# Performance work log

Hardware: AMD Instinct MI355X
Metric: run time of the kernel (lower is better)

The kernel has to match this reference:

```python
import jax, jax.numpy as jnp
import numpy as np

NUM_HEADS = 32
NUM_KV_HEADS = 8
HEAD_DIM = 128
ATTN_SCALE = 0.08838834764831845  # 1/sqrt(128)
CONTEXT_LEN = 8192
BLOCK_SIZE = 16
NUM_BLOCKS = 1024  # physical blocks -> 16384 cache slots


def setup_inputs() -> dict:
    key = jax.random.key(0)
    ks = jax.random.split(key, 6)
    q = jax.random.normal(ks[0], (1, NUM_HEADS, HEAD_DIM), jnp.float32)
    k = jax.random.normal(ks[1], (1, NUM_KV_HEADS, HEAD_DIM), jnp.float32)
    v = jax.random.normal(ks[2], (1, NUM_KV_HEADS, HEAD_DIM), jnp.float32)
    num_slots = NUM_BLOCKS * BLOCK_SIZE
    k_cache = jax.random.normal(ks[3], (num_slots, NUM_KV_HEADS, HEAD_DIM), jnp.float32)
    v_cache = jax.random.normal(ks[4], (num_slots, NUM_KV_HEADS, HEAD_DIM), jnp.float32)
    num_logical = CONTEXT_LEN // BLOCK_SIZE
    block_table = jax.random.permutation(ks[5], NUM_BLOCKS)[:num_logical].astype(jnp.int32)
    # new token is written at logical position context_len - 1
    last = CONTEXT_LEN - 1
    slot_mapping = (block_table[last // BLOCK_SIZE] * BLOCK_SIZE + last % BLOCK_SIZE)[None].astype(jnp.int32)
    return {"q": q, "k": k, "v": v, "k_cache": k_cache, "v_cache": v_cache,
            "block_table": block_table, "slot_mapping": slot_mapping,
            "context_len": CONTEXT_LEN, "block_size": BLOCK_SIZE}


def reference(q, k, v, k_cache, v_cache, block_table, slot_mapping, context_len, block_size):
    # _write_to_cache: scatter the new token's K/V into the paged cache
    k_cache = k_cache.at[slot_mapping].set(k)
    v_cache = v_cache.at[slot_mapping].set(v)
    # _build_full_slot_mapping + _read_from_cache: gather full context K/V
    pos = jnp.arange(context_len)
    slots = block_table[pos // block_size] * block_size + pos % block_size  # (S,)
    k_all = k_cache[slots]  # (S, Hkv, D)
    v_all = v_cache[slots]
    # GQA: repeat_interleave KV heads to match query heads
    g = NUM_HEADS // NUM_KV_HEADS
    k_all = jnp.repeat(k_all, g, axis=1)  # (S, H, D)
    v_all = jnp.repeat(v_all, g, axis=1)
    # manual masked SDPA; num_query_tokens == 1 -> mask is all-ones (no tril)
    scores = jnp.einsum('qhd,khd->hqk', q, k_all) * ATTN_SCALE  # (H, 1, S)
    weights = jax.nn.softmax(scores, axis=-1)
    out = jnp.einsum('hqk,khd->qhd', weights, v_all)  # (1, H, D)
    return out
```

## Files before the change

### kernel.cpp

```cpp
#include <hip/hip_runtime.h>
#include <math.h>


#define NUM_HEADS    32
#define NUM_KV_HEADS 8
#define GQA          4
#define HEAD_DIM     128
#define ATTN_SCALE   0.08838834764831845f
#define CTX          8192
#define BLK          16
#define SPLITS       256
#define HALVES       16
#define SG           8
#define SPS          (SPLITS / SG)

template<int CTRL>
__device__ __forceinline__ float dpp_add(float x) {
    int xi = __builtin_bit_cast(int, x);
    int yi = __builtin_amdgcn_update_dpp(xi, xi, CTRL, 0xF, 0xF, true);
    return x + __builtin_bit_cast(float, yi);
}
__device__ __forceinline__ float swz_add_x16(float x) {
    int yi = __builtin_amdgcn_ds_swizzle(__builtin_bit_cast(int, x), 0x401F);
    return x + __builtin_bit_cast(float, yi);
}
__device__ __forceinline__ float half_wave_sum(float s) {
    s = dpp_add<0xB1>(s);
    s = dpp_add<0x4E>(s);
    s = dpp_add<0x124>(s);
    s = dpp_add<0x128>(s);
    s = swz_add_x16(s);
    return s;
}

__global__ __launch_bounds__(512, 4) void attn_partial(
    const float* __restrict__ q,
    const float* __restrict__ knew,
    const float* __restrict__ vnew,
    const float* __restrict__ kc,
    const float* __restrict__ vc,
    const int*   __restrict__ bt,
    float*       __restrict__ o_part,
    float*       __restrict__ l_part)
{
    const int split = blockIdx.x;
    const int kvh   = blockIdx.y;
    const int tid   = threadIdx.x;
    const int halfid = tid >> 5;
    const int l      = tid & 31;

    const int b0 = bt[split * 2];
    const int b1 = bt[split * 2 + 1];

    float4 qf[GQA];
#pragma unroll
    for (int h = 0; h < GQA; ++h)
        qf[h] = *(const float4*)(q + (kvh * GQA + h) * HEAD_DIM + l * 4);

    float4 kf[2], vf[2];
#pragma unroll
    for (int j = 0; j < 2; ++j) {
        const int off = halfid * 2 + j;
        const int pg  = (off >> 4) ? b1 : b0;
        const float* kptr;
        const float* vptr;
        if (split == SPLITS - 1 && off == 31) {
            kptr = knew + kvh * HEAD_DIM;
            vptr = vnew + kvh * HEAD_DIM;
        } else {
            const size_t row = (((size_t)pg * BLK + (off & 15)) * NUM_KV_HEADS + kvh)
                               * HEAD_DIM;
            kptr = kc + row;
            vptr = vc + row;
        }
        kf[j] = *(const float4*)(kptr + l * 4);
        vf[j] = *(const float4*)(vptr + l * 4);
    }

    float s[2][GQA];
#pragma unroll
    for (int j = 0; j < 2; ++j)
#pragma unroll
        for (int h = 0; h < GQA; ++h)
            s[j][h] = qf[h].x * kf[j].x + qf[h].y * kf[j].y +
                      qf[h].z * kf[j].z + qf[h].w * kf[j].w;

#pragma unroll
    for (int j = 0; j < 2; ++j)
#pragma unroll
        for (int h = 0; h < GQA; ++h)
            s[j][h] = half_wave_sum(s[j][h]);

    float  lsum[GQA];
    float4 o[GQA];
#pragma unroll
    for (int h = 0; h < GQA; ++h) {
        const float p0 = __expf(s[0][h] * ATTN_SCALE);
        const float p1 = __expf(s[1][h] * ATTN_SCALE);
        lsum[h] = p0 + p1;
        o[h].x = p0 * vf[0].x + p1 * vf[1].x;
        o[h].y = p0 * vf[0].y + p1 * vf[1].y;
        o[h].z = p0 * vf[0].z + p1 * vf[1].z;
        o[h].w = p0 * vf[0].w + p1 * vf[1].w;
    }

    __shared__ float  lds_o[HALVES][GQA][HEAD_DIM];
    __shared__ float4 lds_l[HALVES];

#pragma unroll
    for (int h = 0; h < GQA; ++h)
        *(float4*)&lds_o[halfid][h][l * 4] = o[h];
    if (l == 0)
        lds_l[halfid] = make_float4(lsum[0], lsum[1], lsum[2], lsum[3]);
    __syncthreads();

    if (tid < HEAD_DIM) {
        const int d = tid;
#pragma unroll
        for (int h = 0; h < GQA; ++h) {
            float acc = 0.f;
#pragma unroll
            for (int i = 0; i < HALVES; ++i) acc += lds_o[i][h][d];
            o_part[((size_t)(kvh * GQA + h) * SPLITS + split) * HEAD_DIM + d] = acc;
        }
    } else if (tid < 128 + GQA) {
        const int h = tid - 128;
        const float* lp = (const float*)lds_l;
        float L = 0.f;
#pragma unroll
        for (int i = 0; i < HALVES; ++i) L += lp[i * 4 + h];
        l_part[(kvh * GQA + h) * SPLITS + split] = L;
    }
}

__global__ __launch_bounds__(128) void attn_reduce1(
    const float* __restrict__ o_part,
    const float* __restrict__ l_part,
    float*       __restrict__ o2,
    float*       __restrict__ l2)
{
    const int h  = blockIdx.x;
    const int sg = blockIdx.y;
    const int d  = threadIdx.x;
    const int s0 = sg * SPS;

    float acc = 0.f;
#pragma unroll 8
    for (int s = 0; s < SPS; ++s)
        acc += o_part[((size_t)h * SPLITS + s0 + s) * HEAD_DIM + d];
    o2[((size_t)h * SG + sg) * HEAD_DIM + d] = acc;

    if (d < SPS) {
        float lv = l_part[h * SPLITS + s0 + d];
#pragma unroll
        for (int off = 16; off >= 1; off >>= 1) lv += __shfl_xor(lv, off, 64);
        if (d == 0) l2[h * SG + sg] = lv;
    }
}

__global__ __launch_bounds__(128) void attn_reduce2(
    const float* __restrict__ o2,
    const float* __restrict__ l2,
    float*       __restrict__ out)
{
    const int h = blockIdx.x;
    const int d = threadIdx.x;

    float L = 0.f;
#pragma unroll
    for (int i = 0; i < SG; ++i) L += l2[h * SG + i];

    float acc = 0.f;
#pragma unroll
    for (int i = 0; i < SG; ++i)
        acc += o2[((size_t)h * SG + i) * HEAD_DIM + d];

    out[h * HEAD_DIM + d] = acc / L;
}

extern "C" void kernel_launch(void* const* d_in, const int* in_sizes, int n_in,
                              void* d_out, int out_size, void* d_ws, size_t ws_size,
                              hipStream_t stream) {
    const float* q    = (const float*)d_in[0];
    const float* knew = (const float*)d_in[1];
    const float* vnew = (const float*)d_in[2];
    const float* kc   = (const float*)d_in[3];
    const float* vc   = (const float*)d_in[4];
    const int*   bt   = (const int*)d_in[5];

    char* ws = (char*)d_ws;
    float* o_part = (float*)ws;
    ws += (size_t)NUM_HEADS * SPLITS * HEAD_DIM * sizeof(float);
    float* l_part = (float*)ws;
    ws += (size_t)NUM_HEADS * SPLITS * sizeof(float);
    float* o2     = (float*)ws;
    ws += (size_t)NUM_HEADS * SG * HEAD_DIM * sizeof(float);
    float* l2     = (float*)ws;

    attn_partial<<<dim3(SPLITS, NUM_KV_HEADS), 512, 0, stream>>>(
        q, knew, vnew, kc, vc, bt, o_part, l_part);
    attn_reduce1<<<dim3(NUM_HEADS, SG), 128, 0, stream>>>(o_part, l_part, o2, l2);
    attn_reduce2<<<NUM_HEADS, 128, 0, stream>>>(o2, l2, (float*)d_out);
}
```

Baseline: 150.0 us.

## Halve split count with 8 tokens per half-wave and merge reduction kernels

The partial kernel now uses 128 splits of 256 threads, with each 32-lane group processing 8 tokens instead of 2 and accumulating the softmax-weighted values in registers. The two reduction kernels become one 512-thread finish kernel that sums the partial outputs and normalizers in a single launch. This cuts the partial-output traffic and removes one kernel launch. The cost is more registers per thread and fewer blocks available to hide memory latency. Like the code before, it applies exp without subtracting the max, relying on the score range staying small.

```diff
diff --git a/kernel.cpp b/kernel.cpp
--- a/kernel.cpp
+++ b/kernel.cpp
@@ -9,10 +9,9 @@
 #define ATTN_SCALE   0.08838834764831845f
 #define CTX          8192
 #define BLK          16
-#define SPLITS       256
-#define HALVES       16
-#define SG           8
-#define SPS          (SPLITS / SG)
+#define SPLITS       128
+#define HALVES       8
+#define TPH          8
 
 template<int CTRL>
 __device__ __forceinline__ float dpp_add(float x) {
@@ -33,7 +32,7 @@
     return s;
 }
 
-__global__ __launch_bounds__(512, 4) void attn_partial(
+__global__ __launch_bounds__(256, 3) void attn_partial(
     const float* __restrict__ q,
     const float* __restrict__ knew,
     const float* __restrict__ vnew,
@@ -43,65 +42,75 @@
     float*       __restrict__ o_part,
     float*       __restrict__ l_part)
 {
-    const int split = blockIdx.x;
-    const int kvh   = blockIdx.y;
-    const int tid   = threadIdx.x;
+    const int split  = blockIdx.x;
+    const int kvh    = blockIdx.y;
+    const int tid    = threadIdx.x;
     const int halfid = tid >> 5;
     const int l      = tid & 31;
 
-    const int b0 = bt[split * 2];
-    const int b1 = bt[split * 2 + 1];
+    const int tb = split * (HALVES * TPH) + halfid * TPH;
+    const int pg = bt[tb >> 4];
+    const int po = tb & (BLK - 1);
 
     float4 qf[GQA];
 #pragma unroll
     for (int h = 0; h < GQA; ++h)
         qf[h] = *(const float4*)(q + (kvh * GQA + h) * HEAD_DIM + l * 4);
 
-    float4 kf[2], vf[2];
+    const size_t row0 =
+        (((size_t)pg * BLK + po) * NUM_KV_HEADS + kvh) * HEAD_DIM + l * 4;
+    const bool lastHalf = (split == SPLITS - 1) && (halfid == HALVES - 1);
+
+    float4 kf[TPH], vf[TPH];
 #pragma unroll
-    for (int j = 0; j < 2; ++j) {
-        const int off = halfid * 2 + j;
-        const int pg  = (off >> 4) ? b1 : b0;
-        const float* kptr;
-        const float* vptr;
-        if (split == SPLITS - 1 && off == 31) {
-            kptr = knew + kvh * HEAD_DIM;
-            vptr = vnew + kvh * HEAD_DIM;
-        } else {
-            const size_t row = (((size_t)pg * BLK + (off & 15)) * NUM_KV_HEADS + kvh)
-                               * HEAD_DIM;
-            kptr = kc + row;
-            vptr = vc + row;
+    for (int j = 0; j < TPH; ++j) {
+        const float* kp = kc + row0 + (size_t)j * (NUM_KV_HEADS * HEAD_DIM);
+        const float* vp = vc + row0 + (size_t)j * (NUM_KV_HEADS * HEAD_DIM);
+        if (lastHalf && j == TPH - 1) {
+            kp = knew + kvh * HEAD_DIM + l * 4;
+            vp = vnew + kvh * HEAD_DIM + l * 4;
         }
-        kf[j] = *(const float4*)(kptr + l * 4);
-        vf[j] = *(const float4*)(vptr + l * 4);
+        kf[j] = *(const float4*)kp;
+        vf[j] = *(const float4*)vp;
     }
 
-    float s[2][GQA];
+    float4 o[GQA];
+    float  lsum[GQA];
 #pragma unroll
-    for (int j = 0; j < 2; ++j)
-#pragma unroll
-        for (int h = 0; h < GQA; ++h)
-            s[j][h] = qf[h].x * kf[j].x + qf[h].y * kf[j].y +
-                      qf[h].z * kf[j].z + qf[h].w * kf[j].w;
+    for (int h = 0; h < GQA; ++h) {
+        o[h] = make_float4(0.f, 0.f, 0.f, 0.f);
+        lsum[h] = 0.f;
+    }
 
 #pragma unroll
-    for (int j = 0; j < 2; ++j)
+    for (int c = 0; c < 2; ++c) {
+        float s[4][GQA];
 #pragma unroll
-        for (int h = 0; h < GQA; ++h)
-            s[j][h] = half_wave_sum(s[j][h]);
-
-    float  lsum[GQA];
-    float4 o[GQA];
+        for (int jj = 0; jj < 4; ++jj) {
+            const int j = c * 4 + jj;
 #pragma unroll
-    for (int h = 0; h < GQA; ++h) {
-        const float p0 = __expf(s[0][h] * ATTN_SCALE);
-        const float p1 = __expf(s[1][h] * ATTN_SCALE);
-        lsum[h] = p0 + p1;
-        o[h].x = p0 * vf[0].x + p1 * vf[1].x;
-        o[h].y = p0 * vf[0].y + p1 * vf[1].y;
-        o[h].z = p0 * vf[0].z + p1 * vf[1].z;
-        o[h].w = p0 * vf[0].w + p1 * vf[1].w;
+            for (int h = 0; h < GQA; ++h)
+                s[jj][h] = qf[h].x * kf[j].x + qf[h].y * kf[j].y +
+                           qf[h].z * kf[j].z + qf[h].w * kf[j].w;
+        }
+#pragma unroll
+        for (int jj = 0; jj < 4; ++jj)
+#pragma unroll
+            for (int h = 0; h < GQA; ++h)
+                s[jj][h] = half_wave_sum(s[jj][h]);
+#pragma unroll
+        for (int jj = 0; jj < 4; ++jj) {
+            const int j = c * 4 + jj;
+#pragma unroll
+            for (int h = 0; h < GQA; ++h) {
+                const float p = __expf(s[jj][h] * ATTN_SCALE);
+                lsum[h] += p;
+                o[h].x += p * vf[j].x;
+                o[h].y += p * vf[j].y;
+                o[h].z += p * vf[j].z;
+                o[h].w += p * vf[j].w;
+            }
+        }
     }
 
     __shared__ float  lds_o[HALVES][GQA][HEAD_DIM];
@@ -123,8 +132,8 @@
             for (int i = 0; i < HALVES; ++i) acc += lds_o[i][h][d];
             o_part[((size_t)(kvh * GQA + h) * SPLITS + split) * HEAD_DIM + d] = acc;
         }
-    } else if (tid < 128 + GQA) {
-        const int h = tid - 128;
+    } else if (tid < HEAD_DIM + GQA) {
+        const int h = tid - HEAD_DIM;
         const float* lp = (const float*)lds_l;
         float L = 0.f;
 #pragma unroll
@@ -133,49 +142,36 @@
     }
 }
 
-__global__ __launch_bounds__(128) void attn_reduce1(
+__global__ __launch_bounds__(512) void attn_finish(
     const float* __restrict__ o_part,
     const float* __restrict__ l_part,
-    float*       __restrict__ o2,
-    float*       __restrict__ l2)
+    float*       __restrict__ out)
 {
-    const int h  = blockIdx.x;
-    const int sg = blockIdx.y;
-    const int d  = threadIdx.x;
-    const int s0 = sg * SPS;
+    const int h   = blockIdx.x;
+    const int tid = threadIdx.x;
+    const int d   = tid & (HEAD_DIM - 1);
+    const int p   = tid >> 7;
 
     float acc = 0.f;
 #pragma unroll 8
-    for (int s = 0; s < SPS; ++s)
-        acc += o_part[((size_t)h * SPLITS + s0 + s) * HEAD_DIM + d];
-    o2[((size_t)h * SG + sg) * HEAD_DIM + d] = acc;
+    for (int s = 0; s < SPLITS / 4; ++s)
+        acc += o_part[((size_t)h * SPLITS + p * (SPLITS / 4) + s) * HEAD_DIM + d];
 
-    if (d < SPS) {
-        float lv = l_part[h * SPLITS + s0 + d];
+    __shared__ float lds[4][HEAD_DIM];
+    __shared__ float lwave[8];
+    lds[p][d] = acc;
+
+    float lv = 0.f;
+    if (tid < SPLITS) lv = l_part[h * SPLITS + tid];
 #pragma unroll
-        for (int off = 16; off >= 1; off >>= 1) lv += __shfl_xor(lv, off, 64);
-        if (d == 0) l2[h * SG + sg] = lv;
+    for (int off = 32; off >= 1; off >>= 1) lv += __shfl_xor(lv, off, 64);
+    if ((tid & 63) == 0) lwave[tid >> 6] = lv;
+    __syncthreads();
+
+    if (tid < HEAD_DIM) {
+        const float L = lwave[0] + lwave[1];
+        out[h * HEAD_DIM + d] = (lds[0][d] + lds[1][d] + lds[2][d] + lds[3][d]) / L;
     }
-}
-
-__global__ __launch_bounds__(128) void attn_reduce2(
-    const float* __restrict__ o2,
-    const float* __restrict__ l2,
-    float*       __restrict__ out)
-{
-    const int h = blockIdx.x;
-    const int d = threadIdx.x;
-
-    float L = 0.f;
-#pragma unroll
-    for (int i = 0; i < SG; ++i) L += l2[h * SG + i];
-
-    float acc = 0.f;
-#pragma unroll
-    for (int i = 0; i < SG; ++i)
-        acc += o2[((size_t)h * SG + i) * HEAD_DIM + d];
-
-    out[h * HEAD_DIM + d] = acc / L;
 }
 
 extern "C" void kernel_launch(void* const* d_in, const int* in_sizes, int n_in,
@@ -188,17 +184,10 @@
     const float* vc   = (const float*)d_in[4];
     const int*   bt   = (const int*)d_in[5];
 
-    char* ws = (char*)d_ws;
-    float* o_part = (float*)ws;
-    ws += (size_t)NUM_HEADS * SPLITS * HEAD_DIM * sizeof(float);
-    float* l_part = (float*)ws;
-    ws += (size_t)NUM_HEADS * SPLITS * sizeof(float);
-    float* o2     = (float*)ws;
-    ws += (size_t)NUM_HEADS * SG * HEAD_DIM * sizeof(float);
-    float* l2     = (float*)ws;
+    float* o_part = (float*)d_ws;
+    float* l_part = o_part + (size_t)NUM_HEADS * SPLITS * HEAD_DIM;
 
-    attn_partial<<<dim3(SPLITS, NUM_KV_HEADS), 512, 0, stream>>>(
+    attn_partial<<<dim3(SPLITS, NUM_KV_HEADS), 256, 0, stream>>>(
         q, knew, vnew, kc, vc, bt, o_part, l_part);
-    attn_reduce1<<<dim3(NUM_HEADS, SG), 128, 0, stream>>>(o_part, l_part, o2, l2);
-    attn_reduce2<<<NUM_HEADS, 128, 0, stream>>>(o2, l2, (float*)d_out);
+    attn_finish<<<NUM_HEADS, 512, 0, stream>>>(o_part, l_part, (float*)d_out);
 }
```

Measured after the change: 152.8 us. No clear change (+1.9%).
